# Kernel optimization log

Hardware: AMD Instinct MI355X
Metric: run time of the kernel (lower is better)

Reference implementation:

```python
import jax, jax.numpy as jnp
import numpy as np

DECAY = 0.99
EPSILON = 1e-05
N_TOKENS = 32768
EMBED_DIM = 256
NUM_EMB = 4096


def setup_inputs() -> dict:
    key = jax.random.key(0)
    k1, k2, k3 = jax.random.split(key, 3)
    return {
        "inputs": jax.random.normal(k1, (N_TOKENS, EMBED_DIM), dtype=jnp.float32),
        "codebook": jax.random.normal(k2, (NUM_EMB, EMBED_DIM), dtype=jnp.float32),
        "ema_w": jax.random.normal(k3, (NUM_EMB, EMBED_DIM), dtype=jnp.float32),
        "ema_cluster_size": jnp.zeros((NUM_EMB,), dtype=jnp.float32),
    }


def reference(inputs, codebook, ema_w, ema_cluster_size):
    K, D = codebook.shape
    flat = inputs.reshape(-1, D)  # [N, D]
    distances = (
        jnp.sum(flat * flat, axis=1, keepdims=True)
        + jnp.sum(codebook * codebook, axis=1)
        - 2.0 * flat @ codebook.T
    )
    encoding_indices = jnp.argmin(distances, axis=1)  # [N]
    encodings = jax.nn.one_hot(encoding_indices, K, dtype=flat.dtype)  # [N, K]
    quantized = codebook[encoding_indices].reshape(inputs.shape)  # [N, D]

    # EMA update (training branch). dw = encodings.T @ flat expressed as a
    # segment sum to avoid a second [N,K]-sized contraction pass.
    dw = jax.ops.segment_sum(flat, encoding_indices, num_segments=K)  # [K, D]
    counts = jax.ops.segment_sum(
        jnp.ones((flat.shape[0],), dtype=flat.dtype), encoding_indices, num_segments=K
    )  # [K]
    new_ema_w = ema_w * DECAY + (1.0 - DECAY) * dw
    cs = ema_cluster_size * DECAY + (1.0 - DECAY) * counts
    n = jnp.sum(cs)
    cs = (cs + EPSILON) / (n + K * EPSILON) * n  # laplace smoothing
    new_codebook = new_ema_w / cs[:, None]
    return quantized, encodings, new_codebook, new_ema_w, cs
```

## Files before the change

### kernel.cpp

```cpp
#include <hip/hip_runtime.h>
#include <hip/hip_bf16.h>

#define NTOK 32768
#define KEMB 4096
#define DDIM 256
#define DECAYF 0.99f
#define EPSF 1e-5f
#define KSPLIT 256
#define FLAG_THETA 0.09f
#define PRUNE_MARGIN 0.25f

#define B_AHAT  0ull
#define B_BHAT  16777216ull
#define B_PART  18874368ull
#define B_CE    52428800ull
#define B_CNTI  52445184ull
#define B_CSP   52461568ull
#define B_OFFS  52477952ull
#define B_NPTR  52494336ull
#define B_TIDX  52494400ull
#define B_SLOT  52756544ull
#define B_TLIST 52887616ull
#define B_DW    53018688ull

#define OFF_Q  0ull
#define OFF_E  8388608ull
#define OFF_CB 142606336ull
#define OFF_W  143654912ull
#define OFF_CS 144703488ull

typedef __attribute__((ext_vector_type(8))) _Float16 f16x8;
typedef __attribute__((ext_vector_type(4))) _Float16 f16x4;
typedef __attribute__((ext_vector_type(4))) float f32x4;

__global__ __launch_bounds__(256) void prep_kernel(const float* __restrict__ xg,
                                                   const float* __restrict__ cbg,
                                                   _Float16* __restrict__ Ahat,
                                                   _Float16* __restrict__ Bhat,
                                                   float* __restrict__ ce,
                                                   int* __restrict__ countsI,
                                                   float4* __restrict__ dwv) {
    int b = blockIdx.x;
    int tid = threadIdx.x;
    if (b < 4096) {
        size_t gid = (size_t)b * 256 + tid;
        const float* sp = xg + gid * 8;
        f16x8 v;
        #pragma unroll
        for (int t = 0; t < 8; ++t) v[t] = (_Float16)sp[t];
        *(f16x8*)(Ahat + gid * 8) = v;
    } else if (b < 5120) {
        int k = (b - 4096) * 4 + (tid >> 6);
        int lane = tid & 63;
        float4 v = *(const float4*)(cbg + (size_t)k * DDIM + lane * 4);
        f16x4 h;
        h[0] = (_Float16)v.x; h[1] = (_Float16)v.y;
        h[2] = (_Float16)v.z; h[3] = (_Float16)v.w;
        *(f16x4*)(Bhat + (size_t)k * DDIM + lane * 4) = h;
        float s = v.x * v.x + v.y * v.y + v.z * v.z + v.w * v.w;
        #pragma unroll
        for (int o = 32; o > 0; o >>= 1) s += __shfl_down(s, o);
        if (lane == 0) ce[k] = s;
    } else if (b < 5136) {
        countsI[(b - 5120) * 256 + tid] = 0;
    } else {
        float4 z = {0.f, 0.f, 0.f, 0.f};
        dwv[(size_t)(b - 5136) * 256 + tid] = z;
    }
}

__global__ __launch_bounds__(256) void gemm_argmin_kernel(
        const _Float16* __restrict__ Ahat,
        const _Float16* __restrict__ Bhat,
        const float* __restrict__ ceg,
        float4* __restrict__ part) {
    __shared__ _Float16 As[128 * 64];
    __shared__ _Float16 Bs[128 * 64];
    const int tid  = threadIdx.x;
    const int lane = tid & 63;
    const int wave = tid >> 6;
    const int wm = wave >> 1, wn = wave & 1;

    int lin = blockIdx.y * 32 + blockIdx.x;
    lin = (lin & 7) * 1024 + (lin >> 3);
    const int nb = lin & 31, mb = lin >> 5;

    const int col = lane & 15, q = lane >> 4;
    const int cswz = q ^ (col & 7);

    const int srow = tid >> 3;
    const int sswz = (tid & 7) ^ (srow & 7);
    const _Float16* ag = Ahat + (size_t)(mb * 128 + srow) * KSPLIT + sswz * 8;
    const _Float16* bg = Bhat + (size_t)(nb * 128 + srow) * KSPLIT + sswz * 8;

    f32x4 zero = {0.f, 0.f, 0.f, 0.f};
    f32x4 acc[4][4];
    #pragma unroll
    for (int i = 0; i < 4; ++i)
        #pragma unroll
        for (int j = 0; j < 4; ++j) acc[i][j] = zero;

    for (int kt = 0; kt < KSPLIT / 64; ++kt) {
        __syncthreads();
        #pragma unroll
        for (int n = 0; n < 4; ++n) {
            __builtin_amdgcn_global_load_lds(
                (const __attribute__((address_space(1))) void*)(ag + (size_t)n * 32 * KSPLIT + kt * 64),
                (__attribute__((address_space(3))) void*)(As + n * 2048 + tid * 8), 16, 0, 0);
            __builtin_amdgcn_global_load_lds(
                (const __attribute__((address_space(1))) void*)(bg + (size_t)n * 32 * KSPLIT + kt * 64),
                (__attribute__((address_space(3))) void*)(Bs + n * 2048 + tid * 8), 16, 0, 0);
        }
        __syncthreads();

        const f16x8* Av = (const f16x8*)As;
        const f16x8* Bv = (const f16x8*)Bs;
        #pragma unroll
        for (int ks = 0; ks < 2; ++ks) {
            f16x8 a[4], b[4];
            #pragma unroll
            for (int i = 0; i < 4; ++i)
                a[i] = Av[(wm * 64 + i * 16 + col) * 8 + (cswz ^ (ks * 4))];
            #pragma unroll
            for (int j = 0; j < 4; ++j)
                b[j] = Bv[(wn * 64 + j * 16 + col) * 8 + (cswz ^ (ks * 4))];
            #pragma unroll
            for (int i = 0; i < 4; ++i)
                #pragma unroll
                for (int j = 0; j < 4; ++j)
                    acc[i][j] = __builtin_amdgcn_mfma_f32_16x16x32_f16(a[i], b[j], acc[i][j], 0, 0, 0);
        }
    }

    float ce_j[4];
    #pragma unroll
    for (int j = 0; j < 4; ++j) ce_j[j] = ceg[nb * 128 + wn * 64 + j * 16 + col];

    #pragma unroll
    for (int i = 0; i < 4; ++i) {
        #pragma unroll
        for (int r = 0; r < 4; ++r) {
            float b1 = 3.4e38f, b2 = 3.4e38f;
            int i1 = 0x7fffffff;
            #pragma unroll
            for (int j = 0; j < 4; ++j) {
                float s = ce_j[j] - 2.0f * acc[i][j][r];
                int n = nb * 128 + wn * 64 + j * 16 + col;
                if (s < b1) { b2 = b1; b1 = s; i1 = n; }
                else if (s < b2) { b2 = s; }
            }
            #pragma unroll
            for (int m = 1; m < 16; m <<= 1) {
                float ob1 = __shfl_xor(b1, m, 16);
                float ob2 = __shfl_xor(b2, m, 16);
                int   oi  = __shfl_xor(i1, m, 16);
                bool take = (ob1 < b1) || (ob1 == b1 && oi < i1);
                float nb2 = take ? fminf(b1, ob2) : fminf(b2, ob1);
                if (take) { b1 = ob1; i1 = oi; }
                b2 = nb2;
            }
            if (col == i * 4 + r) {
                int mrow = mb * 128 + wm * 64 + i * 16 + q * 4 + r;
                float4 p;
                p.x = b1; p.y = b2; p.z = __int_as_float(i1); p.w = 0.0f;
                part[(size_t)mrow * 64 + nb * 2 + wn] = p;
            }
        }
    }
}

__global__ __launch_bounds__(256) void post_kernel(const float* __restrict__ xg,
                                                   const float* __restrict__ cb,
                                                   const float4* __restrict__ part,
                                                   int* __restrict__ tokIdx,
                                                   int* __restrict__ countsI,
                                                   int* __restrict__ slotOf,
                                                   float* __restrict__ quant,
                                                   float* __restrict__ enc) {
    int row = blockIdx.x * 4 + (threadIdx.x >> 6);
    int lane = threadIdx.x & 63;
    float4 p = part[(size_t)row * 64 + lane];
    float b1 = p.x, b2 = p.y;
    int i1 = __float_as_int(p.z);
    float cb1 = p.x;
    #pragma unroll
    for (int m = 1; m < 64; m <<= 1) {
        float ob1 = __shfl_xor(b1, m);
        float ob2 = __shfl_xor(b2, m);
        int   oi  = __shfl_xor(i1, m);
        bool take = (ob1 < b1) || (ob1 == b1 && oi < i1);
        float nb2 = take ? fminf(b1, ob2) : fminf(b2, ob1);
        if (take) { b1 = ob1; i1 = oi; }
        b2 = nb2;
    }
    int kfin = i1;
    if (b2 - b1 < FLAG_THETA) {
        unsigned long long mask = __ballot(cb1 <= b1 + PRUNE_MARGIN);
        double best = 1e300;
        int bi = 0x7fffffff;
        const float* xr = xg + (size_t)row * DDIM;
        while (mask) {
            int c = __ffsll(mask) - 1;
            mask &= mask - 1;
            int k = c * 64 + lane;
            const float* e = cb + (size_t)k * DDIM;
            double s = 0.0;
            for (int d4 = 0; d4 < DDIM / 4; ++d4) {
                float4 e4 = *(const float4*)(e + d4 * 4);
                float4 x4 = *(const float4*)(xr + d4 * 4);
                double e0 = (double)e4.x, e1 = (double)e4.y;
                double e2 = (double)e4.z, e3 = (double)e4.w;
                s += e0 * (e0 - 2.0 * (double)x4.x) + e1 * (e1 - 2.0 * (double)x4.y)
                   + e2 * (e2 - 2.0 * (double)x4.z) + e3 * (e3 - 2.0 * (double)x4.w);
            }
            if (s < best || (s == best && k < bi)) { best = s; bi = k; }
        }
        #pragma unroll
        for (int m = 1; m < 64; m <<= 1) {
            double ob = __shfl_xor(best, m);
            int   oi  = __shfl_xor(bi, m);
            if (ob < best || (ob == best && oi < bi)) { best = ob; bi = oi; }
        }
        kfin = bi;
    }
    if (lane == 0) {
        tokIdx[row] = kfin;
        slotOf[row] = atomicAdd(countsI + kfin, 1);
        enc[(size_t)row * KEMB + kfin] = 1.0f;
    }
    float4 e = *(const float4*)(cb + (size_t)kfin * DDIM + lane * 4);
    *(float4*)(quant + (size_t)row * DDIM + lane * 4) = e;
}

__global__ __launch_bounds__(256) void scan_cs_kernel(const int* __restrict__ countsI,
                                                      const float* __restrict__ ema_cs,
                                                      int* __restrict__ offs,
                                                      float* __restrict__ cs_pre,
                                                      float* __restrict__ nptr) {
    __shared__ int part[256];
    __shared__ float npart[256];
    __shared__ int pref[257];
    int tid = threadIdx.x;
    int local[16];
    int s = 0;
    float ns = 0.0f;
    #pragma unroll
    for (int i = 0; i < 16; ++i) {
        int c = countsI[tid * 16 + i];
        local[i] = c;
        s += c;
        float csp = ema_cs[tid * 16 + i] * DECAYF + (1.0f - DECAYF) * (float)c;
        cs_pre[tid * 16 + i] = csp;
        ns += csp;
    }
    part[tid] = s;
    npart[tid] = ns;
    __syncthreads();
    if (tid == 0) {
        pref[0] = 0;
        float nn = 0.0f;
        for (int i = 0; i < 256; ++i) {
            pref[i + 1] = pref[i] + part[i];
            nn += npart[i];
        }
        nptr[0] = nn;
    }
    __syncthreads();
    int run = pref[tid];
    #pragma unroll
    for (int i = 0; i < 16; ++i) { offs[tid * 16 + i] = run; run += local[i]; }
}

__global__ __launch_bounds__(256) void filllist_kernel(const int* __restrict__ tokIdx,
                                                       const int* __restrict__ offs,
                                                       const int* __restrict__ slotOf,
                                                       int* __restrict__ tlist) {
    int t = blockIdx.x * 256 + threadIdx.x;
    int k = tokIdx[t];
    tlist[offs[k] + slotOf[t]] = t;
}

#define SEG_CHUNK 32
__global__ __launch_bounds__(256) void segdw_kernel(const float* __restrict__ xg,
                                                    const int* __restrict__ tlist,
                                                    const int* __restrict__ tokIdx,
                                                    float* __restrict__ dw) {
    int tid = threadIdx.x;
    int s0 = blockIdx.x * SEG_CHUNK;
    float acc = 0.0f;
    int curk = -1;
    for (int s = s0; s < s0 + SEG_CHUNK; ++s) {
        int t = tlist[s];
        int k = tokIdx[t];
        if (k != curk) {
            if (curk >= 0) atomicAdd(dw + (size_t)curk * DDIM + tid, acc);
            acc = 0.0f;
            curk = k;
        }
        acc += xg[(size_t)t * DDIM + tid];
    }
    if (curk >= 0) atomicAdd(dw + (size_t)curk * DDIM + tid, acc);
}

__global__ __launch_bounds__(256) void epi_kernel(const float* __restrict__ ema_w,
                                                  const float* __restrict__ dw,
                                                  const float* __restrict__ cs_pre,
                                                  const float* __restrict__ nptr,
                                                  float* __restrict__ new_cb,
                                                  float* __restrict__ new_w,
                                                  float* __restrict__ cs_out) {
    int gid = blockIdx.x * 256 + threadIdx.x;
    int k = gid >> 8, d = gid & 255;
    float n = *nptr;
    float csp = cs_pre[k];
    float cs = (csp + EPSF) / (n + (float)KEMB * EPSF) * n;
    float w = ema_w[gid] * DECAYF + (1.0f - DECAYF) * dw[gid];
    new_w[gid] = w;
    new_cb[gid] = w / cs;
    if (d == 0) cs_out[k] = cs;
}

extern "C" void kernel_launch(void* const* d_in, const int* in_sizes, int n_in,
                              void* d_out, int out_size, void* d_ws, size_t ws_size,
                              hipStream_t stream) {
    const float* xg     = (const float*)d_in[0];
    const float* cbg    = (const float*)d_in[1];
    const float* ema_w  = (const float*)d_in[2];
    const float* ema_cs = (const float*)d_in[3];

    float* out = (float*)d_out;
    unsigned char* wsb = (unsigned char*)d_ws;

    float* quant  = out + OFF_Q;
    float* enc    = out + OFF_E;
    float* new_cb = out + OFF_CB;
    float* new_w  = out + OFF_W;
    float* cs_out = out + OFF_CS;

    _Float16* Ahat = (_Float16*)(wsb + B_AHAT);
    _Float16* Bhat = (_Float16*)(wsb + B_BHAT);
    float4* part   = (float4*)(wsb + B_PART);
    float* ce      = (float*)(wsb + B_CE);
    int*   countsI = (int*)(wsb + B_CNTI);
    float* cs_pre  = (float*)(wsb + B_CSP);
    int*   offs    = (int*)(wsb + B_OFFS);
    float* nptr    = (float*)(wsb + B_NPTR);
    int*   tokIdx  = (int*)(wsb + B_TIDX);
    int*   slotOf  = (int*)(wsb + B_SLOT);
    int*   tlist   = (int*)(wsb + B_TLIST);
    float* dw      = (float*)(wsb + B_DW);

    hipMemsetAsync(enc, 0, (size_t)NTOK * KEMB * sizeof(float), stream);

    prep_kernel<<<6160, 256, 0, stream>>>(xg, cbg, Ahat, Bhat, ce, countsI, (float4*)dw);
    gemm_argmin_kernel<<<dim3(KEMB / 128, NTOK / 128), 256, 0, stream>>>(Ahat, Bhat, ce, part);
    post_kernel<<<NTOK / 4, 256, 0, stream>>>(xg, cbg, part, tokIdx, countsI, slotOf, quant, enc);
    scan_cs_kernel<<<1, 256, 0, stream>>>(countsI, ema_cs, offs, cs_pre, nptr);
    filllist_kernel<<<NTOK / 256, 256, 0, stream>>>(tokIdx, offs, slotOf, tlist);
    segdw_kernel<<<NTOK / SEG_CHUNK, 256, 0, stream>>>(xg, tlist, tokIdx, dw);
    epi_kernel<<<(KEMB * DDIM) / 256, 256, 0, stream>>>(ema_w, dw, cs_pre, nptr,
                                                        new_cb, new_w, cs_out);
}
```

Measured before the change: 804.3 us.

## Pack argmin index into score bits, fuse one-hot write, drop slot array

The GEMM epilogue adds a bias to each distance and packs the column index into the low 6 mantissa bits. Top-2 reduction then becomes plain fmin/fmax with half-width partials (float2 instead of float4), and the chunk index is recovered with a ballot. The separate 512MB memset of the encodings is removed: post_kernel now writes each full one-hot row with vectorized stores. The slotOf array goes away because filllist assigns slots with atomics on offs. Packing loses precision, so the flag and prune thresholds are widened to route more near-ties to the exact double-precision recheck. Atomic slot order makes the segment sum order nondeterministic.

```diff
diff --git a/kernel.cpp b/kernel.cpp
--- a/kernel.cpp
+++ b/kernel.cpp
@@ -7,8 +7,9 @@
 #define DECAYF 0.99f
 #define EPSF 1e-5f
 #define KSPLIT 256
-#define FLAG_THETA 0.09f
-#define PRUNE_MARGIN 0.25f
+#define FLAG_THETA 0.11f
+#define PRUNE_MARGIN 0.28f
+#define SBIAS 4096.0f
 
 #define B_AHAT  0ull
 #define B_BHAT  16777216ull
@@ -19,7 +20,6 @@
 #define B_OFFS  52477952ull
 #define B_NPTR  52494336ull
 #define B_TIDX  52494400ull
-#define B_SLOT  52756544ull
 #define B_TLIST 52887616ull
 #define B_DW    53018688ull
 
@@ -73,7 +73,7 @@
         const _Float16* __restrict__ Ahat,
         const _Float16* __restrict__ Bhat,
         const float* __restrict__ ceg,
-        float4* __restrict__ part) {
+        float2* __restrict__ part) {
     __shared__ _Float16 As[128 * 64];
     __shared__ _Float16 Bs[128 * 64];
     const int tid  = threadIdx.x;
@@ -140,29 +140,28 @@
     for (int i = 0; i < 4; ++i) {
         #pragma unroll
         for (int r = 0; r < 4; ++r) {
-            float b1 = 3.4e38f, b2 = 3.4e38f;
-            int i1 = 0x7fffffff;
+            float p1 = 3.4e38f, p2 = 3.4e38f;
             #pragma unroll
             for (int j = 0; j < 4; ++j) {
-                float s = ce_j[j] - 2.0f * acc[i][j][r];
-                int n = nb * 128 + wn * 64 + j * 16 + col;
-                if (s < b1) { b2 = b1; b1 = s; i1 = n; }
-                else if (s < b2) { b2 = s; }
+                float s = ce_j[j] - 2.0f * acc[i][j][r] + SBIAS;
+                int loc = j * 16 + col;
+                float sp = __int_as_float((__float_as_int(s) & ~63) | loc);
+                if (sp < p1) { p2 = p1; p1 = sp; }
+                else if (sp < p2) { p2 = sp; }
             }
             #pragma unroll
             for (int m = 1; m < 16; m <<= 1) {
-                float ob1 = __shfl_xor(b1, m, 16);
-                float ob2 = __shfl_xor(b2, m, 16);
-                int   oi  = __shfl_xor(i1, m, 16);
-                bool take = (ob1 < b1) || (ob1 == b1 && oi < i1);
-                float nb2 = take ? fminf(b1, ob2) : fminf(b2, ob1);
-                if (take) { b1 = ob1; i1 = oi; }
-                b2 = nb2;
+                float o1 = __shfl_xor(p1, m, 16);
+                float o2 = __shfl_xor(p2, m, 16);
+                float lo = fminf(p1, o1);
+                float hi = fmaxf(p1, o1);
+                p2 = fminf(hi, fminf(p2, o2));
+                p1 = lo;
             }
             if (col == i * 4 + r) {
                 int mrow = mb * 128 + wm * 64 + i * 16 + q * 4 + r;
-                float4 p;
-                p.x = b1; p.y = b2; p.z = __int_as_float(i1); p.w = 0.0f;
+                float2 p;
+                p.x = p1; p.y = p2;
                 part[(size_t)mrow * 64 + nb * 2 + wn] = p;
             }
         }
@@ -171,31 +170,33 @@
 
 __global__ __launch_bounds__(256) void post_kernel(const float* __restrict__ xg,
                                                    const float* __restrict__ cb,
-                                                   const float4* __restrict__ part,
+                                                   const float2* __restrict__ part,
                                                    int* __restrict__ tokIdx,
                                                    int* __restrict__ countsI,
-                                                   int* __restrict__ slotOf,
                                                    float* __restrict__ quant,
                                                    float* __restrict__ enc) {
     int row = blockIdx.x * 4 + (threadIdx.x >> 6);
     int lane = threadIdx.x & 63;
-    float4 p = part[(size_t)row * 64 + lane];
+    float2 p = part[(size_t)row * 64 + lane];
+    float own = p.x;
     float b1 = p.x, b2 = p.y;
-    int i1 = __float_as_int(p.z);
-    float cb1 = p.x;
     #pragma unroll
     for (int m = 1; m < 64; m <<= 1) {
-        float ob1 = __shfl_xor(b1, m);
-        float ob2 = __shfl_xor(b2, m);
-        int   oi  = __shfl_xor(i1, m);
-        bool take = (ob1 < b1) || (ob1 == b1 && oi < i1);
-        float nb2 = take ? fminf(b1, ob2) : fminf(b2, ob1);
-        if (take) { b1 = ob1; i1 = oi; }
-        b2 = nb2;
-    }
-    int kfin = i1;
+        float o1 = __shfl_xor(b1, m);
+        float o2 = __shfl_xor(b2, m);
+        float lo = fminf(b1, o1);
+        float hi = fmaxf(b1, o1);
+        b2 = fminf(hi, fminf(b2, o2));
+        b1 = lo;
+    }
+    int kfin;
+    {
+        unsigned long long wmask = __ballot(own == b1);
+        int wl = __ffsll(wmask) - 1;
+        kfin = wl * 64 + (__float_as_int(b1) & 63);
+    }
     if (b2 - b1 < FLAG_THETA) {
-        unsigned long long mask = __ballot(cb1 <= b1 + PRUNE_MARGIN);
+        unsigned long long mask = __ballot(own <= b1 + PRUNE_MARGIN);
         double best = 1e300;
         int bi = 0x7fffffff;
         const float* xr = xg + (size_t)row * DDIM;
@@ -225,8 +226,18 @@
     }
     if (lane == 0) {
         tokIdx[row] = kfin;
-        slotOf[row] = atomicAdd(countsI + kfin, 1);
-        enc[(size_t)row * KEMB + kfin] = 1.0f;
+        atomicAdd(countsI + kfin, 1);
+    }
+    {
+        float4* er = (float4*)(enc + (size_t)row * KEMB);
+        int kf4 = kfin >> 2, kc = kfin & 3;
+        #pragma unroll
+        for (int v = 0; v < 16; ++v) {
+            int f4 = v * 64 + lane;
+            float4 val = {0.f, 0.f, 0.f, 0.f};
+            if (f4 == kf4) ((float*)&val)[kc] = 1.0f;
+            er[f4] = val;
+        }
     }
     float4 e = *(const float4*)(cb + (size_t)kfin * DDIM + lane * 4);
     *(float4*)(quant + (size_t)row * DDIM + lane * 4) = e;
@@ -272,12 +283,12 @@
 }
 
 __global__ __launch_bounds__(256) void filllist_kernel(const int* __restrict__ tokIdx,
-                                                       const int* __restrict__ offs,
-                                                       const int* __restrict__ slotOf,
+                                                       int* __restrict__ offs,
                                                        int* __restrict__ tlist) {
     int t = blockIdx.x * 256 + threadIdx.x;
     int k = tokIdx[t];
-    tlist[offs[k] + slotOf[t]] = t;
+    int slot = atomicAdd(offs + k, 1);
+    tlist[slot] = t;
 }
 
 #define SEG_CHUNK 32
@@ -339,24 +350,21 @@
 
     _Float16* Ahat = (_Float16*)(wsb + B_AHAT);
     _Float16* Bhat = (_Float16*)(wsb + B_BHAT);
-    float4* part   = (float4*)(wsb + B_PART);
+    float2* part   = (float2*)(wsb + B_PART);
     float* ce      = (float*)(wsb + B_CE);
     int*   countsI = (int*)(wsb + B_CNTI);
     float* cs_pre  = (float*)(wsb + B_CSP);
     int*   offs    = (int*)(wsb + B_OFFS);
     float* nptr    = (float*)(wsb + B_NPTR);
     int*   tokIdx  = (int*)(wsb + B_TIDX);
-    int*   slotOf  = (int*)(wsb + B_SLOT);
     int*   tlist   = (int*)(wsb + B_TLIST);
     float* dw      = (float*)(wsb + B_DW);
 
-    hipMemsetAsync(enc, 0, (size_t)NTOK * KEMB * sizeof(float), stream);
-
     prep_kernel<<<6160, 256, 0, stream>>>(xg, cbg, Ahat, Bhat, ce, countsI, (float4*)dw);
     gemm_argmin_kernel<<<dim3(KEMB / 128, NTOK / 128), 256, 0, stream>>>(Ahat, Bhat, ce, part);
-    post_kernel<<<NTOK / 4, 256, 0, stream>>>(xg, cbg, part, tokIdx, countsI, slotOf, quant, enc);
+    post_kernel<<<NTOK / 4, 256, 0, stream>>>(xg, cbg, part, tokIdx, countsI, quant, enc);
     scan_cs_kernel<<<1, 256, 0, stream>>>(countsI, ema_cs, offs, cs_pre, nptr);
-    filllist_kernel<<<NTOK / 256, 256, 0, stream>>>(tokIdx, offs, slotOf, tlist);
+    filllist_kernel<<<NTOK / 256, 256, 0, stream>>>(tokIdx, offs, tlist);
     segdw_kernel<<<NTOK / SEG_CHUNK, 256, 0, stream>>>(xg, tlist, tokIdx, dw);
     epi_kernel<<<(KEMB * DDIM) / 256, 256, 0, stream>>>(ema_w, dw, cs_pre, nptr,
                                                         new_cb, new_w, cs_out);
```

Result: no change. 797.5 us (-0.8%).
